# Optimization experiments

Measured on AMD Instinct MI355X. Metric: run time of the kernel, lower is better.

The kernel has to match this reference:

```python
import jax, jax.numpy as jnp
import numpy as np

B, N, C = 2, 2048, 256
L, H = 4, 4
HD = C // H  # 64, div=1 so q/k keep full head dim
EPS = 1e-5   # BatchNorm eps (eval mode, running_mean=0, running_var=1)


def setup_inputs() -> dict:
    key = jax.random.key(0)
    ks = jax.random.split(key, 20)
    w = lambda k, s: jax.random.normal(k, s, jnp.float32) * 0.05
    return {
        'x': jax.random.normal(ks[0], (B, N, C), jnp.float32),
        'in_w1': w(ks[1], (C, C)), 'in_b1': w(ks[2], (C,)),
        'in_g1': 1.0 + w(ks[3], (C,)), 'in_be1': w(ks[4], (C,)),
        'in_w2': w(ks[5], (C, C)), 'in_b2': w(ks[6], (C,)),
        'in_g2': 1.0 + w(ks[7], (C,)), 'in_be2': w(ks[8], (C,)),
        'q_w': w(ks[9], (L, H, HD, HD)), 'k_w': w(ks[10], (L, H, HD, HD)),
        'v_w': w(ks[11], (L, H, HD, HD)), 'v_b': w(ks[12], (L, H, HD)),
        't_w': w(ks[13], (L, H, HD, HD)), 't_b': w(ks[14], (L, H, HD)),
        'bn_g': 1.0 + w(ks[15], (L, H, HD)), 'bn_b': w(ks[16], (L, H, HD)),
        'proj_w': w(ks[17], (L, C, C)), 'proj_b': w(ks[18], (L, C)),
    }


def _bn(t, g, b):
    # eval-mode BatchNorm1d with running_mean=0, running_var=1
    return t * (g / jnp.sqrt(1.0 + EPS))[:, None] + b[:, None]


def _forward(x, in_w1, in_b1, in_g1, in_be1, in_w2, in_b2, in_g2, in_be2,
             q_w, k_w, v_w, v_b, t_w, t_b, bn_g, bn_b, proj_w, proj_b):
    Bq, Nq, Cq = x.shape
    h = x.transpose(0, 2, 1)  # (B, C, N)
    h = jax.nn.relu(_bn(jnp.einsum('oc,bcn->bon', in_w1, h) + in_b1[:, None], in_g1, in_be1))
    h = jax.nn.relu(_bn(jnp.einsum('oc,bcn->bon', in_w2, h) + in_b2[:, None], in_g2, in_be2))
    h = h.reshape(Bq, H, HD, Nq)  # split heads (B, H, hd, N)
    for l in range(L):
        xq = jnp.einsum('hoc,bhcn->bhno', q_w[l], h)                       # (B,H,N,hd)
        xk = jnp.einsum('hoc,bhcn->bhon', k_w[l], h)                       # (B,H,hd,N)
        xv = jnp.einsum('hoc,bhcn->bhon', v_w[l], h) + v_b[l][None, :, :, None]
        attn = jax.nn.softmax(jnp.einsum('bhno,bhom->bhnm', xq, xk), axis=-1)
        # offset-attention normalization: divide by column sums (torch dim=1)
        attn = attn / (1e-9 + attn.sum(axis=2, keepdims=True))
        xr = jnp.einsum('bhcn,bhnm->bhcm', xv, attn)                       # (B,H,hd,N)
        d = h - xr
        t = jnp.einsum('hoc,bhcn->bhon', t_w[l], d) + t_b[l][None, :, :, None]
        xr = jax.nn.relu(t * (bn_g[l] / jnp.sqrt(1.0 + EPS))[None, :, :, None]
                         + bn_b[l][None, :, :, None])
        h = h + xr
        hm = h.reshape(Bq, Cq, Nq)  # concat heads
        hm = jnp.einsum('oc,bcn->bon', proj_w[l], hm) + proj_b[l][:, None]
        h = hm.reshape(Bq, H, HD, Nq)
    return h.reshape(Bq, Cq, Nq).transpose(0, 2, 1)  # (B, N, C)


def reference(x, in_w1, in_b1, in_g1, in_be1, in_w2, in_b2, in_g2, in_be2,
              q_w, k_w, v_w, v_b, t_w, t_b, bn_g, bn_b, proj_w, proj_b):
    return _forward(x, in_w1, in_b1, in_g1, in_be1, in_w2, in_b2, in_g2, in_be2,
                    q_w, k_w, v_w, v_b, t_w, t_b, bn_g, bn_b, proj_w, proj_b)
```

## Files before the change

kernel.cpp:

```cpp
#include <hip/hip_runtime.h>
#include <math.h>

constexpr int NB = 2, NN = 2048, NC = 256, NL = 4, NH = 4, ND = 64;
constexpr float EPSV = 1e-5f;

using half8 = __attribute__((ext_vector_type(8))) _Float16;
using half4 = __attribute__((ext_vector_type(4))) _Float16;
using f32x4 = __attribute__((ext_vector_type(4))) float;

__device__ __forceinline__ f32x4 mfma16(half8 a, half8 b, f32x4 c) {
    return __builtin_amdgcn_mfma_f32_16x16x32_f16(a, b, c, 0, 0, 0);
}
__device__ __forceinline__ half8 cvt8(const float* p) {
    float4 x0 = *(const float4*)p, x1 = *(const float4*)(p + 4);
    half8 h;
    h[0]=(_Float16)x0.x; h[1]=(_Float16)x0.y; h[2]=(_Float16)x0.z; h[3]=(_Float16)x0.w;
    h[4]=(_Float16)x1.x; h[5]=(_Float16)x1.y; h[6]=(_Float16)x1.z; h[7]=(_Float16)x1.w;
    return h;
}

template<int EPI, bool INF16, bool OUT32>
__global__ __launch_bounds__(256) void gemm_mfma(
    const float* __restrict__ Wg, const float* __restrict__ bias,
    const float* __restrict__ gam, const float* __restrict__ bet,
    const void* __restrict__ inp, void* __restrict__ outp)
{
    int b = blockIdx.x, o0 = blockIdx.y * 64, n0 = blockIdx.z * 32;
    int t = threadIdx.x, w = t >> 6, li = t & 15, qd = (t >> 4) & 3;
    const float* wr = Wg + (size_t)(o0 + w * 16 + li) * NC + qd * 8;
    half8 af[8];
#pragma unroll
    for (int ks = 0; ks < 8; ++ks) af[ks] = cvt8(wr + ks * 32);
    f32x4 acc[2];
    acc[0] = {0.f, 0.f, 0.f, 0.f}; acc[1] = {0.f, 0.f, 0.f, 0.f};
#pragma unroll
    for (int ks = 0; ks < 8; ++ks) {
#pragma unroll
        for (int g = 0; g < 2; ++g) {
            int n = n0 + g * 16 + li;
            half8 bf;
            if (INF16) {
                bf = *(const half8*)((const _Float16*)inp +
                        ((size_t)(b * NN + n) * NC + ks * 32 + qd * 8));
            } else {
                bf = cvt8((const float*)inp + ((size_t)(b * NN + n) * NC + ks * 32 + qd * 8));
            }
            acc[g] = mfma16(af[ks], bf, acc[g]);
        }
    }
    int ob = o0 + w * 16 + qd * 4;
    float4 bs = *(const float4*)(bias + ob);
    float4 gs = {0,0,0,0}, be = {0,0,0,0};
    if (EPI == 1) { gs = *(const float4*)(gam + ob); be = *(const float4*)(bet + ob); }
    float scl = rsqrtf(1.f + EPSV);
#pragma unroll
    for (int g = 0; g < 2; ++g) {
        int n = n0 + g * 16 + li;
        float v4[4];
#pragma unroll
        for (int r = 0; r < 4; ++r) {
            float v = acc[g][r] + ((const float*)&bs)[r];
            if (EPI == 1)
                v = fmaxf(0.f, v * (((const float*)&gs)[r] * scl) + ((const float*)&be)[r]);
            v4[r] = v;
        }
        if (OUT32) {
            float4 fv = {v4[0], v4[1], v4[2], v4[3]};
            *(float4*)((float*)outp + (size_t)(b * NN + n) * NC + ob) = fv;
        } else {
            half4 hv;
#pragma unroll
            for (int r = 0; r < 4; ++r) hv[r] = (_Float16)v4[r];
            *(half4*)((_Float16*)outp + (size_t)(b * NN + n) * NC + ob) = hv;
        }
    }
}

template<int EPI, bool FINAL>
__global__ __launch_bounds__(256) void proj_qkv(
    const float* __restrict__ Wg, const float* __restrict__ bias,
    const float* __restrict__ gam, const float* __restrict__ bet,
    const _Float16* __restrict__ inp,
    _Float16* __restrict__ h16,
    float* __restrict__ out32,
    const float* __restrict__ qw, const float* __restrict__ kw,
    const float* __restrict__ vw, const float* __restrict__ vb,
    _Float16* __restrict__ q16, _Float16* __restrict__ k16,
    _Float16* __restrict__ v16, int lq)
{
    int bh = blockIdx.x, n0 = blockIdx.y * 32;
    int hh = bh & 3, b = bh >> 2;
    __shared__ __align__(16) _Float16 hp[32][72];
    int t = threadIdx.x, w = t >> 6, li = t & 15, qd = (t >> 4) & 3;

    const float* wr = Wg + (size_t)(hh * 64 + w * 16 + li) * NC + qd * 8;
    half8 af[8];
#pragma unroll
    for (int ks = 0; ks < 8; ++ks) af[ks] = cvt8(wr + ks * 32);
    f32x4 acc[2];
    acc[0] = {0.f, 0.f, 0.f, 0.f}; acc[1] = {0.f, 0.f, 0.f, 0.f};
#pragma unroll
    for (int ks = 0; ks < 8; ++ks) {
#pragma unroll
        for (int g = 0; g < 2; ++g) {
            int n = n0 + g * 16 + li;
            half8 bf = *(const half8*)(inp + ((size_t)(b * NN + n) * NC + ks * 32 + qd * 8));
            acc[g] = mfma16(af[ks], bf, acc[g]);
        }
    }
    int obl = w * 16 + qd * 4;
    int ob = hh * 64 + obl;
    float4 bs = *(const float4*)(bias + ob);
    float4 gs = {0,0,0,0}, be = {0,0,0,0};
    if (EPI == 1) { gs = *(const float4*)(gam + ob); be = *(const float4*)(bet + ob); }
    float scl = rsqrtf(1.f + EPSV);
#pragma unroll
    for (int g = 0; g < 2; ++g) {
        int n = n0 + g * 16 + li;
        float v4[4];
#pragma unroll
        for (int r = 0; r < 4; ++r) {
            float v = acc[g][r] + ((const float*)&bs)[r];
            if (EPI == 1)
                v = fmaxf(0.f, v * (((const float*)&gs)[r] * scl) + ((const float*)&be)[r]);
            v4[r] = v;
        }
        if (FINAL) {
            float4 fv = {v4[0], v4[1], v4[2], v4[3]};
            *(float4*)(out32 + (size_t)(b * NN + n) * NC + ob) = fv;
        } else {
            half4 hv;
#pragma unroll
            for (int r = 0; r < 4; ++r) hv[r] = (_Float16)v4[r];
            *(half4*)(h16 + (size_t)(b * NN + n) * NC + ob) = hv;
            *(half4*)(&hp[g * 16 + li][obl]) = hv;
        }
    }
    if (FINAL) return;
    __syncthreads();

    size_t wbase = (size_t)(lq * NH + hh) * ND * ND;
    size_t wro = (size_t)(w * 16 + li) * ND + qd * 8;
    half8 aq0 = cvt8(qw + wbase + wro), aq1 = cvt8(qw + wbase + wro + 32);
    half8 ak0 = cvt8(kw + wbase + wro), ak1 = cvt8(kw + wbase + wro + 32);
    half8 av0 = cvt8(vw + wbase + wro), av1 = cvt8(vw + wbase + wro + 32);
    f32x4 accq[2], acck[2], accv[2];
#pragma unroll
    for (int g = 0; g < 2; ++g) {
        accq[g] = {0.f,0.f,0.f,0.f}; acck[g] = {0.f,0.f,0.f,0.f}; accv[g] = {0.f,0.f,0.f,0.f};
    }
#pragma unroll
    for (int g = 0; g < 2; ++g) {
        half8 b0 = *(const half8*)(&hp[g * 16 + li][qd * 8]);
        half8 b1 = *(const half8*)(&hp[g * 16 + li][qd * 8 + 32]);
        accq[g] = mfma16(aq0, b0, accq[g]); accq[g] = mfma16(aq1, b1, accq[g]);
        acck[g] = mfma16(ak0, b0, acck[g]); acck[g] = mfma16(ak1, b1, acck[g]);
        accv[g] = mfma16(av0, b0, accv[g]); accv[g] = mfma16(av1, b1, accv[g]);
    }
    int obq = w * 16 + qd * 4;
    _Float16* qo = q16 + (size_t)bh * NN * ND;
    _Float16* ko = k16 + (size_t)bh * NN * ND;
#pragma unroll
    for (int g = 0; g < 2; ++g) {
        int n = n0 + g * 16 + li;
        half4 hq, hk;
#pragma unroll
        for (int r = 0; r < 4; ++r) { hq[r] = (_Float16)accq[g][r]; hk[r] = (_Float16)acck[g][r]; }
        *(half4*)(qo + (size_t)n * ND + obq) = hq;
        *(half4*)(ko + (size_t)n * ND + obq) = hk;
    }
    float4 vb4 = *(const float4*)(vb + (size_t)(lq * NH + hh) * ND + obq);
    _Float16* vo = v16 + (size_t)bh * ND * NN;
#pragma unroll
    for (int g = 0; g < 2; ++g) {
        int n = n0 + g * 16 + li;
#pragma unroll
        for (int r = 0; r < 4; ++r)
            vo[(size_t)(obq + r) * NN + n] = (_Float16)(accv[g][r] + ((const float*)&vb4)[r]);
    }
}

__global__ __launch_bounds__(256) void rowsum_part(
    const _Float16* __restrict__ qh, const _Float16* __restrict__ kh,
    float* __restrict__ rowsum_p)
{
    int bh = blockIdx.x, nt = blockIdx.y, ms = blockIdx.z;
    const _Float16* qp = qh + (size_t)bh * NN * ND;
    const _Float16* kp = kh + (size_t)bh * NN * ND;
    int t = threadIdx.x, w = t >> 6, li = t & 15, qd = (t >> 4) & 3;
    int nr = nt * 64 + w * 16;
    half8 aq0 = *(const half8*)(qp + (size_t)(nr + li) * ND + qd * 8);
    half8 aq1 = *(const half8*)(qp + (size_t)(nr + li) * ND + qd * 8 + 32);
    float rsacc[4] = {0.f, 0.f, 0.f, 0.f};
    for (int it = 0; it < 8; ++it) {
        int m0 = ms * 512 + it * 64;
        f32x4 s[4];
#pragma unroll
        for (int g = 0; g < 4; ++g) {
            const _Float16* kb = kp + (size_t)(m0 + g * 16 + li) * ND + qd * 8;
            half8 b0 = *(const half8*)(kb);
            half8 b1 = *(const half8*)(kb + 32);
            s[g] = {0.f, 0.f, 0.f, 0.f};
            s[g] = mfma16(aq0, b0, s[g]);
            s[g] = mfma16(aq1, b1, s[g]);
        }
#pragma unroll
        for (int r = 0; r < 4; ++r)
            rsacc[r] += __expf(s[0][r]) + __expf(s[1][r]) + __expf(s[2][r]) + __expf(s[3][r]);
    }
#pragma unroll
    for (int r = 0; r < 4; ++r) {
        float v = rsacc[r];
        v += __shfl_xor(v, 1); v += __shfl_xor(v, 2);
        v += __shfl_xor(v, 4); v += __shfl_xor(v, 8);
        if (li == 0) rowsum_p[((size_t)(ms * NB * NH + bh)) * NN + nr + qd * 4 + r] = v;
    }
}

__global__ __launch_bounds__(256) void attn_part(
    const _Float16* __restrict__ qh, const _Float16* __restrict__ kh,
    const _Float16* __restrict__ vh, const float* __restrict__ rowsum_p,
    _Float16* __restrict__ xrp16, float* __restrict__ csp)
{
    int bh = blockIdx.x, m0 = blockIdx.y * 64, ns = blockIdx.z;
    const _Float16* qp = qh + (size_t)bh * NN * ND;
    const _Float16* kp = kh + (size_t)bh * NN * ND;
    const _Float16* vp = vh + (size_t)bh * ND * NN;
    __shared__ __align__(16) _Float16 Plds[2][64 * 72];
    __shared__ float cs_wave[4][64];
    int t = threadIdx.x, w = t >> 6, li = t & 15, qd = (t >> 4) & 3;
    const size_t RSS = (size_t)NB * NH * NN;
    half8 bk[4][2];
#pragma unroll
    for (int g = 0; g < 4; ++g) {
        const _Float16* kb = kp + (size_t)(m0 + g * 16 + li) * ND + qd * 8;
        bk[g][0] = *(const half8*)(kb);
        bk[g][1] = *(const half8*)(kb + 32);
    }
    f32x4 acc[4];
#pragma unroll
    for (int g = 0; g < 4; ++g) acc[g] = {0.f, 0.f, 0.f, 0.f};
    float csacc[4] = {0.f, 0.f, 0.f, 0.f};
    int nb0 = ns * 512;
    const _Float16* qrow0 = qp + (size_t)(nb0 + w * 16 + li) * ND + qd * 8;
    half8 aq0 = *(const half8*)(qrow0);
    half8 aq1 = *(const half8*)(qrow0 + 32);
    int ridx = bh * NN + nb0 + w * 16 + qd * 4;
    float4 r0 = *(const float4*)(rowsum_p + ridx);
    float4 r1 = *(const float4*)(rowsum_p + RSS + ridx);
    float4 r2 = *(const float4*)(rowsum_p + 2 * RSS + ridx);
    float4 r3 = *(const float4*)(rowsum_p + 3 * RSS + ridx);
    for (int it = 0; it < 8; ++it) {
        int n0 = ns * 512 + it * 64;
        _Float16* Pb = Plds[it & 1];
        const _Float16* vrow = vp + (size_t)(w * 16 + li) * NN + n0 + qd * 8;
        half8 av0 = *(const half8*)(vrow);
        half8 av1 = *(const half8*)(vrow + 32);
        f32x4 s[4];
#pragma unroll
        for (int g = 0; g < 4; ++g) {
            s[g] = {0.f, 0.f, 0.f, 0.f};
            s[g] = mfma16(aq0, bk[g][0], s[g]);
            s[g] = mfma16(aq1, bk[g][1], s[g]);
        }
        float irs[4];
        irs[0] = 1.f / (r0.x + r1.x + r2.x + r3.x);
        irs[1] = 1.f / (r0.y + r1.y + r2.y + r3.y);
        irs[2] = 1.f / (r0.z + r1.z + r2.z + r3.z);
        irs[3] = 1.f / (r0.w + r1.w + r2.w + r3.w);
        if (it < 7) {
            const _Float16* nqrow = qp + (size_t)(n0 + 64 + w * 16 + li) * ND + qd * 8;
            aq0 = *(const half8*)(nqrow);
            aq1 = *(const half8*)(nqrow + 32);
            int nridx = bh * NN + n0 + 64 + w * 16 + qd * 4;
            r0 = *(const float4*)(rowsum_p + nridx);
            r1 = *(const float4*)(rowsum_p + RSS + nridx);
            r2 = *(const float4*)(rowsum_p + 2 * RSS + nridx);
            r3 = *(const float4*)(rowsum_p + 3 * RSS + nridx);
        }
#pragma unroll
        for (int g = 0; g < 4; ++g) {
            half4 pv; float lsum = 0.f;
#pragma unroll
            for (int r = 0; r < 4; ++r) {
                float p = __expf(s[g][r]) * irs[r];
                lsum += p;
                pv[r] = (_Float16)p;
            }
            csacc[g] += lsum;
            *(half4*)(&Pb[(g * 16 + li) * 72 + w * 16 + qd * 4]) = pv;
        }
        __syncthreads();
#pragma unroll
        for (int g = 0; g < 4; ++g) {
            half8 b0 = *(const half8*)(&Pb[(g * 16 + li) * 72 + qd * 8]);
            half8 b1 = *(const half8*)(&Pb[(g * 16 + li) * 72 + qd * 8 + 32]);
            acc[g] = mfma16(av0, b0, acc[g]);
            acc[g] = mfma16(av1, b1, acc[g]);
        }
    }
#pragma unroll
    for (int g = 0; g < 4; ++g) {
        float v = csacc[g];
        v += __shfl_xor(v, 16); v += __shfl_xor(v, 32);
        if (qd == 0) cs_wave[w][g * 16 + li] = v;
    }
    __syncthreads();
    if (t < 64) {
        float cs = cs_wave[0][t] + cs_wave[1][t] + cs_wave[2][t] + cs_wave[3][t];
        csp[((size_t)ns * NB * NH + bh) * NN + m0 + t] = cs;
    }
    _Float16* xo = xrp16 + (size_t)ns * ((size_t)NB * NC * NN);
#pragma unroll
    for (int g = 0; g < 4; ++g)
#pragma unroll
        for (int r = 0; r < 4; ++r)
            xo[(size_t)(bh * 64 + w * 16 + qd * 4 + r) * NN + m0 + g * 16 + li] =
                (_Float16)acc[g][r];
}

__global__ __launch_bounds__(256) void delta_fused(
    const float* __restrict__ tw, const float* __restrict__ tb,
    const float* __restrict__ bng, const float* __restrict__ bnb,
    const _Float16* __restrict__ xrp16, const float* __restrict__ csp,
    const _Float16* __restrict__ h16, _Float16* __restrict__ hn16, int l)
{
    int bh = blockIdx.x, n0 = blockIdx.y * 32;
    int hh = bh & 3, b = bh >> 2;
    __shared__ float xt[64][33];
    int t = threadIdx.x;
    {
        int xcol = t & 31, yr = t >> 5;
        int m = n0 + xcol;
        const size_t CSS = (size_t)NB * NH * NN;
        float cs = 1e-9f;
#pragma unroll
        for (int sl = 0; sl < 4; ++sl) cs += csp[sl * CSS + (size_t)bh * NN + m];
        float icv = 1.f / cs;
        const size_t XSS = (size_t)NB * NC * NN;
#pragma unroll
        for (int r = 0; r < 8; ++r) {
            int c = yr + 8 * r;
            size_t off = (size_t)(bh * 64 + c) * NN + m;
            float s = 0.f;
#pragma unroll
            for (int sl = 0; sl < 4; ++sl) s += (float)xrp16[sl * XSS + off];
            xt[c][xcol] = s * icv;
        }
    }
    __syncthreads();
    int w = t >> 6, li = t & 15, qd = (t >> 4) & 3;
    const float* wp = tw + (size_t)(l * NH + hh) * ND * ND;
    const float* wr = wp + (size_t)(w * 16 + li) * ND + qd * 8;
    half8 af0 = cvt8(wr), af1 = cvt8(wr + 32);
    f32x4 acc[2];
    acc[0] = {0.f, 0.f, 0.f, 0.f}; acc[1] = {0.f, 0.f, 0.f, 0.f};
#pragma unroll
    for (int g = 0; g < 2; ++g) {
        int nl = g * 16 + li;
        size_t hoff = (size_t)(b * NN + n0 + nl) * NC + hh * 64;
        half8 h0 = *(const half8*)(h16 + hoff + qd * 8);
        half8 h1 = *(const half8*)(h16 + hoff + 32 + qd * 8);
        half8 b0, b1;
#pragma unroll
        for (int j = 0; j < 8; ++j) {
            b0[j] = (_Float16)((float)h0[j] - xt[qd * 8 + j][nl]);
            b1[j] = (_Float16)((float)h1[j] - xt[32 + qd * 8 + j][nl]);
        }
        acc[g] = mfma16(af0, b0, acc[g]);
        acc[g] = mfma16(af1, b1, acc[g]);
    }
    int ob = w * 16 + qd * 4;
    float4 tb4 = *(const float4*)(tb  + (size_t)(l * NH + hh) * ND + ob);
    float4 g4  = *(const float4*)(bng + (size_t)(l * NH + hh) * ND + ob);
    float4 b4  = *(const float4*)(bnb + (size_t)(l * NH + hh) * ND + ob);
    float scl = rsqrtf(1.f + EPSV);
#pragma unroll
    for (int g = 0; g < 2; ++g) {
        int n = n0 + g * 16 + li;
        size_t off = (size_t)(b * NN + n) * NC + hh * 64 + ob;
        half4 h4 = *(const half4*)(h16 + off);
        half4 hv;
#pragma unroll
        for (int r = 0; r < 4; ++r) {
            float tv = acc[g][r] + ((const float*)&tb4)[r];
            float x2 = fmaxf(0.f, tv * (((const float*)&g4)[r] * scl) + ((const float*)&b4)[r]);
            hv[r] = (_Float16)((float)h4[r] + x2);
        }
        *(half4*)(hn16 + off) = hv;
    }
}

extern "C" void kernel_launch(void* const* d_in, const int* in_sizes, int n_in,
                              void* d_out, int out_size, void* d_ws, size_t ws_size,
                              hipStream_t stream)
{
    (void)in_sizes; (void)n_in; (void)out_size; (void)ws_size;
    const float* x      = (const float*)d_in[0];
    const float* in_w1  = (const float*)d_in[1];
    const float* in_b1  = (const float*)d_in[2];
    const float* in_g1  = (const float*)d_in[3];
    const float* in_be1 = (const float*)d_in[4];
    const float* in_w2  = (const float*)d_in[5];
    const float* in_b2  = (const float*)d_in[6];
    const float* in_g2  = (const float*)d_in[7];
    const float* in_be2 = (const float*)d_in[8];
    const float* q_w    = (const float*)d_in[9];
    const float* k_w    = (const float*)d_in[10];
    const float* v_w    = (const float*)d_in[11];
    const float* v_b    = (const float*)d_in[12];
    const float* t_w    = (const float*)d_in[13];
    const float* t_b    = (const float*)d_in[14];
    const float* bn_g   = (const float*)d_in[15];
    const float* bn_b   = (const float*)d_in[16];
    const float* proj_w = (const float*)d_in[17];
    const float* proj_b = (const float*)d_in[18];

    float* ws = (float*)d_ws;
    const size_t M = (size_t)NB * NC * NN;
    float* rowsum_p = ws;
    float* csp      = ws + 65536;
    _Float16* xrp16 = (_Float16*)(ws + 131072);
    _Float16* hbase = (_Float16*)(ws + 131072 + 2 * M);
    _Float16* h16  = hbase;
    _Float16* hA16 = hbase + M;
    _Float16* q16  = hbase + 2 * M;
    _Float16* k16  = hbase + 3 * M;
    _Float16* v16  = hbase + 4 * M;

    dim3 g1(NB, NC / 64, NN / 32);
    dim3 gf(NB * NH, NN / 32);

    gemm_mfma<1, false, false><<<g1, 256, 0, stream>>>(in_w1, in_b1, in_g1, in_be1, x, hA16);
    proj_qkv<1, false><<<gf, 256, 0, stream>>>(
        in_w2, in_b2, in_g2, in_be2, hA16, h16, nullptr,
        q_w, k_w, v_w, v_b, q16, k16, v16, 0);

    for (int l = 0; l < NL; l++) {
        rowsum_part<<<dim3(NB * NH, NN / 64, 4), 256, 0, stream>>>(q16, k16, rowsum_p);
        attn_part<<<dim3(NB * NH, NN / 64, 4), 256, 0, stream>>>(
            q16, k16, v16, rowsum_p, xrp16, csp);
        delta_fused<<<dim3(NB * NH, NN / 32), 256, 0, stream>>>(
            t_w, t_b, bn_g, bn_b, xrp16, csp, h16, hA16, l);
        if (l < NL - 1) {
            proj_qkv<0, false><<<gf, 256, 0, stream>>>(
                proj_w + (size_t)l * NC * NC, proj_b + (size_t)l * NC,
                nullptr, nullptr, hA16, h16, nullptr,
                q_w, k_w, v_w, v_b, q16, k16, v16, l + 1);
        } else {
            proj_qkv<0, true><<<gf, 256, 0, stream>>>(
                proj_w + (size_t)l * NC * NC, proj_b + (size_t)l * NC,
                nullptr, nullptr, hA16, nullptr, (float*)d_out,
                q_w, k_w, v_w, v_b, q16, k16, v16, 0);
        }
    }
}
```

Before: 424.6 us.

## Keep softmax probabilities in registers and feed them directly to k16 MFMA in attention

Restructures attn_part so each wave owns a 32-column slice of m and a 256-row half of the n range, computing S with K32 MFMA and then feeding the exponentiated probabilities straight from the accumulator layout into 16x16x16 MFMAs as the B operand. This removes the per-iteration LDS round-trip and __syncthreads for P. The two n-halves are reduced at the end through a shared-memory buffer. The cost is more accumulator registers, smaller per-instruction MFMA work, and per-step uncoalesced 8-byte V loads from global memory.

```diff
diff --git a/kernel.cpp b/kernel.cpp
--- a/kernel.cpp
+++ b/kernel.cpp
@@ -10,6 +10,9 @@
 
 __device__ __forceinline__ f32x4 mfma16(half8 a, half8 b, f32x4 c) {
     return __builtin_amdgcn_mfma_f32_16x16x32_f16(a, b, c, 0, 0, 0);
+}
+__device__ __forceinline__ f32x4 mfma16k16(half4 a, half4 b, f32x4 c) {
+    return __builtin_amdgcn_mfma_f32_16x16x16f16(a, b, c, 0, 0, 0);
 }
 __device__ __forceinline__ half8 cvt8(const float* p) {
     float4 x0 = *(const float4*)p, x1 = *(const float4*)(p + 4);
@@ -226,97 +229,123 @@
     const _Float16* qp = qh + (size_t)bh * NN * ND;
     const _Float16* kp = kh + (size_t)bh * NN * ND;
     const _Float16* vp = vh + (size_t)bh * ND * NN;
-    __shared__ __align__(16) _Float16 Plds[2][64 * 72];
-    __shared__ float cs_wave[4][64];
+    __shared__ float red[64][68];
+    __shared__ float cs_w[2][64];
     int t = threadIdx.x, w = t >> 6, li = t & 15, qd = (t >> 4) & 3;
+    int wn = w & 1, wm = w >> 1;
     const size_t RSS = (size_t)NB * NH * NN;
-    half8 bk[4][2];
-#pragma unroll
-    for (int g = 0; g < 4; ++g) {
-        const _Float16* kb = kp + (size_t)(m0 + g * 16 + li) * ND + qd * 8;
+
+    half8 bk[2][2];
+#pragma unroll
+    for (int g = 0; g < 2; ++g) {
+        const _Float16* kb = kp + (size_t)(m0 + wm * 32 + g * 16 + li) * ND + qd * 8;
         bk[g][0] = *(const half8*)(kb);
         bk[g][1] = *(const half8*)(kb + 32);
     }
-    f32x4 acc[4];
-#pragma unroll
-    for (int g = 0; g < 4; ++g) acc[g] = {0.f, 0.f, 0.f, 0.f};
-    float csacc[4] = {0.f, 0.f, 0.f, 0.f};
-    int nb0 = ns * 512;
-    const _Float16* qrow0 = qp + (size_t)(nb0 + w * 16 + li) * ND + qd * 8;
-    half8 aq0 = *(const half8*)(qrow0);
-    half8 aq1 = *(const half8*)(qrow0 + 32);
-    int ridx = bh * NN + nb0 + w * 16 + qd * 4;
-    float4 r0 = *(const float4*)(rowsum_p + ridx);
-    float4 r1 = *(const float4*)(rowsum_p + RSS + ridx);
-    float4 r2 = *(const float4*)(rowsum_p + 2 * RSS + ridx);
-    float4 r3 = *(const float4*)(rowsum_p + 3 * RSS + ridx);
-    for (int it = 0; it < 8; ++it) {
-        int n0 = ns * 512 + it * 64;
-        _Float16* Pb = Plds[it & 1];
-        const _Float16* vrow = vp + (size_t)(w * 16 + li) * NN + n0 + qd * 8;
-        half8 av0 = *(const half8*)(vrow);
-        half8 av1 = *(const half8*)(vrow + 32);
-        f32x4 s[4];
-#pragma unroll
-        for (int g = 0; g < 4; ++g) {
+    f32x4 acc[4][2];
+#pragma unroll
+    for (int cs = 0; cs < 4; ++cs)
+#pragma unroll
+        for (int g = 0; g < 2; ++g) acc[cs][g] = {0.f, 0.f, 0.f, 0.f};
+    float csacc[2] = {0.f, 0.f};
+
+    const int nw = ns * 512 + wn * 256;
+    const _Float16* qr = qp + (size_t)(nw + li) * ND + qd * 8;
+    half8 aq0 = *(const half8*)(qr);
+    half8 aq1 = *(const half8*)(qr + 32);
+    float4 irs;
+    {
+        int ridx = bh * NN + nw + qd * 4;
+        float4 r0 = *(const float4*)(rowsum_p + ridx);
+        float4 r1 = *(const float4*)(rowsum_p + RSS + ridx);
+        float4 r2 = *(const float4*)(rowsum_p + 2 * RSS + ridx);
+        float4 r3 = *(const float4*)(rowsum_p + 3 * RSS + ridx);
+        irs.x = 1.f / (r0.x + r1.x + r2.x + r3.x);
+        irs.y = 1.f / (r0.y + r1.y + r2.y + r3.y);
+        irs.z = 1.f / (r0.z + r1.z + r2.z + r3.z);
+        irs.w = 1.f / (r0.w + r1.w + r2.w + r3.w);
+    }
+    half4 vf[4];
+#pragma unroll
+    for (int cs = 0; cs < 4; ++cs)
+        vf[cs] = *(const half4*)(vp + (size_t)(cs * 16 + li) * NN + nw + qd * 4);
+
+    for (int it = 0; it < 16; ++it) {
+        half8 caq0 = aq0, caq1 = aq1;
+        float4 cirs = irs;
+        half4 cvf[4] = {vf[0], vf[1], vf[2], vf[3]};
+        if (it < 15) {
+            int nb = nw + (it + 1) * 16;
+            const _Float16* nqr = qp + (size_t)(nb + li) * ND + qd * 8;
+            aq0 = *(const half8*)(nqr);
+            aq1 = *(const half8*)(nqr + 32);
+            int ridx = bh * NN + nb + qd * 4;
+            float4 r0 = *(const float4*)(rowsum_p + ridx);
+            float4 r1 = *(const float4*)(rowsum_p + RSS + ridx);
+            float4 r2 = *(const float4*)(rowsum_p + 2 * RSS + ridx);
+            float4 r3 = *(const float4*)(rowsum_p + 3 * RSS + ridx);
+            irs.x = 1.f / (r0.x + r1.x + r2.x + r3.x);
+            irs.y = 1.f / (r0.y + r1.y + r2.y + r3.y);
+            irs.z = 1.f / (r0.z + r1.z + r2.z + r3.z);
+            irs.w = 1.f / (r0.w + r1.w + r2.w + r3.w);
+#pragma unroll
+            for (int cs = 0; cs < 4; ++cs)
+                vf[cs] = *(const half4*)(vp + (size_t)(cs * 16 + li) * NN + nb + qd * 4);
+        }
+        f32x4 s[2];
+#pragma unroll
+        for (int g = 0; g < 2; ++g) {
             s[g] = {0.f, 0.f, 0.f, 0.f};
-            s[g] = mfma16(aq0, bk[g][0], s[g]);
-            s[g] = mfma16(aq1, bk[g][1], s[g]);
-        }
-        float irs[4];
-        irs[0] = 1.f / (r0.x + r1.x + r2.x + r3.x);
-        irs[1] = 1.f / (r0.y + r1.y + r2.y + r3.y);
-        irs[2] = 1.f / (r0.z + r1.z + r2.z + r3.z);
-        irs[3] = 1.f / (r0.w + r1.w + r2.w + r3.w);
-        if (it < 7) {
-            const _Float16* nqrow = qp + (size_t)(n0 + 64 + w * 16 + li) * ND + qd * 8;
-            aq0 = *(const half8*)(nqrow);
-            aq1 = *(const half8*)(nqrow + 32);
-            int nridx = bh * NN + n0 + 64 + w * 16 + qd * 4;
-            r0 = *(const float4*)(rowsum_p + nridx);
-            r1 = *(const float4*)(rowsum_p + RSS + nridx);
-            r2 = *(const float4*)(rowsum_p + 2 * RSS + nridx);
-            r3 = *(const float4*)(rowsum_p + 3 * RSS + nridx);
-        }
-#pragma unroll
-        for (int g = 0; g < 4; ++g) {
-            half4 pv; float lsum = 0.f;
+            s[g] = mfma16(caq0, bk[g][0], s[g]);
+            s[g] = mfma16(caq1, bk[g][1], s[g]);
+        }
+#pragma unroll
+        for (int g = 0; g < 2; ++g) {
+            half4 p; float lsum = 0.f;
 #pragma unroll
             for (int r = 0; r < 4; ++r) {
-                float p = __expf(s[g][r]) * irs[r];
-                lsum += p;
-                pv[r] = (_Float16)p;
+                float pv = __expf(s[g][r]) * ((const float*)&cirs)[r];
+                lsum += pv;
+                p[r] = (_Float16)pv;
             }
             csacc[g] += lsum;
-            *(half4*)(&Pb[(g * 16 + li) * 72 + w * 16 + qd * 4]) = pv;
-        }
-        __syncthreads();
-#pragma unroll
-        for (int g = 0; g < 4; ++g) {
-            half8 b0 = *(const half8*)(&Pb[(g * 16 + li) * 72 + qd * 8]);
-            half8 b1 = *(const half8*)(&Pb[(g * 16 + li) * 72 + qd * 8 + 32]);
-            acc[g] = mfma16(av0, b0, acc[g]);
-            acc[g] = mfma16(av1, b1, acc[g]);
-        }
-    }
-#pragma unroll
-    for (int g = 0; g < 4; ++g) {
+#pragma unroll
+            for (int cs = 0; cs < 4; ++cs)
+                acc[cs][g] = mfma16k16(cvf[cs], p, acc[cs][g]);
+        }
+    }
+
+#pragma unroll
+    for (int g = 0; g < 2; ++g) {
         float v = csacc[g];
         v += __shfl_xor(v, 16); v += __shfl_xor(v, 32);
-        if (qd == 0) cs_wave[w][g * 16 + li] = v;
+        if (qd == 0) cs_w[wn][wm * 32 + g * 16 + li] = v;
+    }
+    if (wn == 0) {
+#pragma unroll
+        for (int cs = 0; cs < 4; ++cs)
+#pragma unroll
+            for (int g = 0; g < 2; ++g)
+#pragma unroll
+                for (int r = 0; r < 4; ++r)
+                    red[cs * 16 + qd * 4 + r][wm * 32 + g * 16 + li] = acc[cs][g][r];
     }
     __syncthreads();
-    if (t < 64) {
-        float cs = cs_wave[0][t] + cs_wave[1][t] + cs_wave[2][t] + cs_wave[3][t];
-        csp[((size_t)ns * NB * NH + bh) * NN + m0 + t] = cs;
-    }
     _Float16* xo = xrp16 + (size_t)ns * ((size_t)NB * NC * NN);
-#pragma unroll
-    for (int g = 0; g < 4; ++g)
-#pragma unroll
-        for (int r = 0; r < 4; ++r)
-            xo[(size_t)(bh * 64 + w * 16 + qd * 4 + r) * NN + m0 + g * 16 + li] =
-                (_Float16)acc[g][r];
+    if (wn == 1) {
+#pragma unroll
+        for (int cs = 0; cs < 4; ++cs)
+#pragma unroll
+            for (int g = 0; g < 2; ++g)
+#pragma unroll
+                for (int r = 0; r < 4; ++r) {
+                    int c = cs * 16 + qd * 4 + r, ml = wm * 32 + g * 16 + li;
+                    float sum = acc[cs][g][r] + red[c][ml];
+                    xo[(size_t)(bh * 64 + c) * NN + m0 + ml] = (_Float16)sum;
+                }
+    }
+    if (t < 64)
+        csp[((size_t)ns * NB * NH + bh) * NN + m0 + t] = cs_w[0][t] + cs_w[1][t];
 }
 
 __global__ __launch_bounds__(256) void delta_fused(
```

Measured after the change: 535.3 us. 1.26x slower.
